# Kernel tuning notes

Hardware: AMD Instinct MI355X
Metric: run time of the kernel (lower is better)

## Reference

```python
import jax, jax.numpy as jnp
import numpy as np

N_NODES = 100000
N_EDGES = 1600000
IN_C, HID_C, OUT_C = 512, 128, 40


def gcn_conv(x, edge_index):
    """Symmetric-normalized sparse aggregation: out[d] = sum_e 1/sqrt(deg[s]*deg[d]) * x[s]."""
    n = x.shape[0]
    src, dst = edge_index[0], edge_index[1]
    deg = jax.ops.segment_sum(jnp.ones_like(dst, dtype=x.dtype), dst, num_segments=n)
    deg = jnp.maximum(deg, 1.0)  # guard isolated nodes
    dinv = jax.lax.rsqrt(deg)
    w = dinv[src] * dinv[dst]                      # [E]
    msg = x[src] * w[:, None]                      # [E, C] gather + scale
    return jax.ops.segment_sum(msg, dst, num_segments=n)  # scatter-add -> [N, C]


def setup_inputs() -> dict:
    key = jax.random.key(0)
    k1, k2, k3, k4 = jax.random.split(key, 4)
    x = jax.random.normal(k1, (N_NODES, IN_C), dtype=jnp.float32)
    edge_index = jax.random.randint(k2, (2, N_EDGES), 0, N_NODES, dtype=jnp.int64)
    # xavier_uniform with gain=1.414 (as in reset_parameters), zero biases
    def xavier(k, shape, gain=1.414):
        fan_out, fan_in = shape
        bound = gain * np.sqrt(6.0 / (fan_in + fan_out))
        return jax.random.uniform(k, shape, jnp.float32, -bound, bound)
    W0 = xavier(k3, (HID_C, IN_C))
    b0 = jnp.zeros((HID_C,), jnp.float32)
    W1 = xavier(k4, (OUT_C, HID_C))
    b1 = jnp.zeros((OUT_C,), jnp.float32)
    return {"x": x, "edge_index": edge_index, "W0": W0, "b0": b0, "W1": W1, "b1": b1}


def reference(x, edge_index, W0, b0, W1, b1):
    # layer 0: project -> sparse aggregate -> bias -> relu (dropout off in eval)
    h = x @ W0.T
    h = gcn_conv(h, edge_index)
    h = jax.nn.relu(h + b0)
    # final layer: project -> sparse aggregate -> bias (no activation)
    h = h @ W1.T
    h = gcn_conv(h, edge_index)
    return h + b1
```

## Files before the change

### kernel.cpp

```cpp
#include <hip/hip_runtime.h>
#include <hip/hip_bf16.h>
#include <cstddef>

#define N_NODES 100000
#define N_EDGES 1600000
#define IN_C 512
#define HID_C 128
#define OUT_C 40
#define OUT_CP 48
#define BK 128
#define PADK 136
#define EPB 8000
#define NPART 200
#define NBKT 196
#define BSHIFT 9

typedef short bf16x8 __attribute__((ext_vector_type(8)));
typedef float f32x4 __attribute__((ext_vector_type(4)));

__device__ __forceinline__ float bf2f(unsigned short u) {
    union { unsigned int i; float f; } v; v.i = ((unsigned int)u) << 16; return v.f;
}
__device__ __forceinline__ float bf2f_lo(unsigned int u) {
    union { unsigned int i; float f; } v; v.i = u << 16; return v.f;
}
__device__ __forceinline__ float bf2f_hi(unsigned int u) {
    union { unsigned int i; float f; } v; v.i = u & 0xFFFF0000u; return v.f;
}
__device__ __forceinline__ unsigned short f2bf(float f) {
    union { float f; unsigned int i; } v; v.f = f;
    unsigned int x = v.i;
    return (unsigned short)((x + 0x7FFFu + ((x >> 16) & 1u)) >> 16);
}

__device__ __forceinline__ void glds16(const void* g, void* l) {
    __builtin_amdgcn_global_load_lds(
        (const __attribute__((address_space(1))) unsigned int*)g,
        (__attribute__((address_space(3))) unsigned int*)l,
        16, 0, 0);
}

__global__ void k_detect(const unsigned int* __restrict__ xbits,
                         const int* __restrict__ ei32, int* __restrict__ flags) {
    if (threadIdx.x == 0 && blockIdx.x == 0) {
        int inrange = 0;
        for (int i = 0; i < 64; i++) {
            unsigned int b = xbits[i * 33 + 1];
            int e = (int)((b >> 23) & 0xFFu);
            if (e >= 90 && e <= 160) inrange++;
        }
        flags[0] = (inrange >= 32) ? 0 : 1;
        int zeros = 0;
        for (int i = 0; i < 8; i++) if (ei32[2 * i + 1] == 0) zeros++;
        flags[1] = (zeros == 8) ? 1 : 0;
    }
}

__device__ __forceinline__ int load_src(const int* ei, int mi, int e) {
    return mi ? ei[2 * e] : ei[e];
}
__device__ __forceinline__ int load_dst(const int* ei, int mi, int e) {
    return mi ? ei[2 * (N_EDGES + e)] : ei[N_EDGES + e];
}

#define NW_TOTAL (IN_C * HID_C + HID_C * OUT_C + HID_C + OUT_C)
__global__ void k_norm_w(const void* __restrict__ W0, const void* __restrict__ W1,
                         const void* __restrict__ b0, const void* __restrict__ b1,
                         const int* __restrict__ flags,
                         unsigned short* __restrict__ w0n, unsigned short* __restrict__ w1n,
                         float* __restrict__ b0n, float* __restrict__ b1n) {
    int mf = flags[0];
    int i = blockIdx.x * 256 + threadIdx.x;
    if (i >= NW_TOTAL) return;
    if (i < IN_C * HID_C) {
        w0n[i] = mf ? ((const unsigned short*)W0)[i] : f2bf(((const float*)W0)[i]);
    } else if (i < IN_C * HID_C + HID_C * OUT_C) {
        int j = i - IN_C * HID_C;
        w1n[j] = mf ? ((const unsigned short*)W1)[j] : f2bf(((const float*)W1)[j]);
    } else if (i < IN_C * HID_C + HID_C * OUT_C + HID_C) {
        int j = i - IN_C * HID_C - HID_C * OUT_C;
        b0n[j] = mf ? bf2f(((const unsigned short*)b0)[j]) : ((const float*)b0)[j];
    } else {
        int j = i - IN_C * HID_C - HID_C * OUT_C - HID_C;
        b1n[j] = mf ? bf2f(((const unsigned short*)b1)[j]) : ((const float*)b1)[j];
    }
}

__global__ __launch_bounds__(256) void k_part1(const int* __restrict__ ei,
                                               const int* __restrict__ flags,
                                               int* __restrict__ bcnt,
                                               int* __restrict__ block_off) {
    __shared__ int h[NBKT];
    int t = threadIdx.x;
    for (int i = t; i < NBKT; i += 256) h[i] = 0;
    __syncthreads();
    int mi = flags[1];
    int base = blockIdx.x * EPB;
    for (int j = t; j < EPB; j += 256) {
        int e = base + j;
        if (e < N_EDGES) atomicAdd(&h[load_dst(ei, mi, e) >> BSHIFT], 1);
    }
    __syncthreads();
    for (int i = t; i < NBKT; i += 256)
        block_off[blockIdx.x * NBKT + i] = atomicAdd(&bcnt[i], h[i]);
}

__global__ void k_scan_bkt(const int* __restrict__ bcnt, int* __restrict__ bbase) {
    __shared__ int sm[256];
    int t = threadIdx.x;
    int v = (t < NBKT) ? bcnt[t] : 0;
    sm[t] = v; __syncthreads();
    for (int off = 1; off < 256; off <<= 1) {
        int a = (t >= off) ? sm[t - off] : 0;
        __syncthreads();
        sm[t] += a;
        __syncthreads();
    }
    if (t < NBKT) bbase[t] = sm[t] - v;
    if (t == NBKT - 1) bbase[NBKT] = sm[t];
}

__global__ __launch_bounds__(256) void k_part2(const int* __restrict__ ei,
                                               const int* __restrict__ flags,
                                               const int* __restrict__ bbase,
                                               const int* __restrict__ block_off,
                                               unsigned int* __restrict__ bedges) {
    __shared__ int cur[NBKT];
    int t = threadIdx.x;
    for (int i = t; i < NBKT; i += 256)
        cur[i] = bbase[i] + block_off[blockIdx.x * NBKT + i];
    __syncthreads();
    int mi = flags[1];
    int base = blockIdx.x * EPB;
    for (int j = t; j < EPB; j += 256) {
        int e = base + j;
        if (e < N_EDGES) {
            int d = load_dst(ei, mi, e);
            int s = load_src(ei, mi, e);
            int p = atomicAdd(&cur[d >> BSHIFT], 1);
            bedges[p] = ((unsigned int)s << BSHIFT) | (unsigned int)(d & 511);
        }
    }
}

__global__ __launch_bounds__(512) void k_bucket_csr(const unsigned int* __restrict__ bedges,
                                                    const int* __restrict__ bbase,
                                                    int* __restrict__ rowptr,
                                                    float* __restrict__ dinv,
                                                    int* __restrict__ col) {
    __shared__ int cnt[512];
    __shared__ int cur[512];
    int b = blockIdx.x, t = threadIdx.x;
    int ebeg = bbase[b], eend = bbase[b + 1];
    cnt[t] = 0;
    __syncthreads();
    for (int j = ebeg + t; j < eend; j += 512)
        atomicAdd(&cnt[bedges[j] & 511], 1);
    __syncthreads();
    int v = cnt[t];
    cur[t] = v; __syncthreads();
    for (int off = 1; off < 512; off <<= 1) {
        int a = (t >= off) ? cur[t - off] : 0;
        __syncthreads();
        cur[t] += a;
        __syncthreads();
    }
    int excl = cur[t] - v;
    int node = b * 512 + t;
    if (node < N_NODES) {
        rowptr[node] = ebeg + excl;
        float dd = (float)v; if (dd < 1.f) dd = 1.f;
        dinv[node] = rsqrtf(dd);
    } else if (node == N_NODES) {
        rowptr[N_NODES] = ebeg + excl;
    }
    __syncthreads();
    cur[t] = ebeg + excl;
    __syncthreads();
    for (int j = ebeg + t; j < eend; j += 512) {
        unsigned int pk = bedges[j];
        int p = atomicAdd(&cur[pk & 511], 1);
        col[p] = (int)(pk >> BSHIFT);
    }
}

template <int MF>
__device__ __forceinline__ void gemm1_body(const void* __restrict__ x,
                                           const unsigned short* __restrict__ w0n,
                                           unsigned short* __restrict__ h1,
                                           unsigned short* __restrict__ Bl,
                                           int node0, int t) {
    int w = t >> 6;
    int lane = t & 63;
    int r16 = lane & 15;
    int quad = lane >> 4;

    f32x4 acc[2][8];
#pragma unroll
    for (int m = 0; m < 2; m++)
#pragma unroll
        for (int c = 0; c < 8; c++) acc[m][c] = (f32x4){0.f, 0.f, 0.f, 0.f};

    int row0 = node0 + w * 32 + r16;
    int row1 = row0 + 16;
    int r0c = row0 < N_NODES ? row0 : N_NODES - 1;
    int r1c = row1 < N_NODES ? row1 : N_NODES - 1;
    const float* a0f = (const float*)x + (size_t)r0c * IN_C + quad * 8;
    const float* a1f = (const float*)x + (size_t)r1c * IN_C + quad * 8;
    const unsigned short* a0h = (const unsigned short*)x + (size_t)r0c * IN_C + quad * 8;
    const unsigned short* a1h = (const unsigned short*)x + (size_t)r1c * IN_C + quad * 8;

    int ch = t >> 1, half = t & 1;
    const unsigned short* gfill = w0n + (size_t)ch * IN_C + half * 64;
    unsigned short* lfill = Bl + ch * PADK + half * 64;

    for (int s = 0; s < 4; s++) {
        int ks0 = s * BK;
        __syncthreads();
#pragma unroll
        for (int i = 0; i < 8; i++) {
            *reinterpret_cast<bf16x8*>(lfill + i * 8) =
                *reinterpret_cast<const bf16x8*>(gfill + ks0 + i * 8);
        }
        __syncthreads();
#pragma unroll
        for (int kk = 0; kk < BK; kk += 32) {
            int k0 = ks0 + kk;
            bf16x8 a0, a1;
            if (MF) {
                a0 = *reinterpret_cast<const bf16x8*>(a0h + k0);
                a1 = *reinterpret_cast<const bf16x8*>(a1h + k0);
            } else {
                float4 f0 = *reinterpret_cast<const float4*>(a0f + k0);
                float4 f1 = *reinterpret_cast<const float4*>(a0f + k0 + 4);
                float4 g0 = *reinterpret_cast<const float4*>(a1f + k0);
                float4 g1 = *reinterpret_cast<const float4*>(a1f + k0 + 4);
                a0 = (bf16x8){(short)f2bf(f0.x), (short)f2bf(f0.y), (short)f2bf(f0.z), (short)f2bf(f0.w),
                              (short)f2bf(f1.x), (short)f2bf(f1.y), (short)f2bf(f1.z), (short)f2bf(f1.w)};
                a1 = (bf16x8){(short)f2bf(g0.x), (short)f2bf(g0.y), (short)f2bf(g0.z), (short)f2bf(g0.w),
                              (short)f2bf(g1.x), (short)f2bf(g1.y), (short)f2bf(g1.z), (short)f2bf(g1.w)};
            }
            const unsigned short* bbase2 = Bl + r16 * PADK + kk + quad * 8;
#pragma unroll
            for (int ct = 0; ct < 8; ct++) {
                bf16x8 b = *reinterpret_cast<const bf16x8*>(bbase2 + ct * 16 * PADK);
                acc[0][ct] = __builtin_amdgcn_mfma_f32_16x16x32_bf16(a0, b, acc[0][ct], 0, 0, 0);
                acc[1][ct] = __builtin_amdgcn_mfma_f32_16x16x32_bf16(a1, b, acc[1][ct], 0, 0, 0);
            }
        }
    }

#pragma unroll
    for (int m = 0; m < 2; m++) {
#pragma unroll
        for (int ct = 0; ct < 8; ct++) {
#pragma unroll
            for (int r = 0; r < 4; r++) {
                int row = node0 + w * 32 + m * 16 + quad * 4 + r;
                if (row < N_NODES)
                    h1[(size_t)row * HID_C + ct * 16 + r16] = f2bf(acc[m][ct][r]);
            }
        }
    }
}

__device__ __forceinline__ void gemm1_bf16_async(const unsigned short* __restrict__ xg,
                                                 const unsigned short* __restrict__ w0n,
                                                 unsigned short* __restrict__ h1,
                                                 unsigned short* __restrict__ smem,
                                                 int node0, int t) {
    const int w = t >> 6;
    const int lane = t & 63;
    const int r16 = lane & 15;
    const int quad = lane >> 4;

    f32x4 acc[2][8];
#pragma unroll
    for (int m = 0; m < 2; m++)
#pragma unroll
        for (int c = 0; c < 8; c++) acc[m][c] = (f32x4){0.f, 0.f, 0.f, 0.f};

    int rA0 = node0 + (2 * w) * 16 + r16;     if (rA0 >= N_NODES) rA0 = N_NODES - 1;
    int rA1 = node0 + (2 * w + 1) * 16 + r16; if (rA1 >= N_NODES) rA1 = N_NODES - 1;
    const unsigned short* pa0 = xg + (size_t)rA0 * IN_C + quad * 8;
    const unsigned short* pa1 = xg + (size_t)rA1 * IN_C + quad * 8;
    const unsigned short* pb0 = w0n + (size_t)((2 * w) * 16 + r16) * IN_C + quad * 8;
    const unsigned short* pb1 = w0n + (size_t)((2 * w + 1) * 16 + r16) * IN_C + quad * 8;

    auto stage = [&](int buf, int ks) {
        unsigned short* a = smem + buf * 8192 + (2 * w) * 512;
        glds16(pa0 + ks, a);
        glds16(pa1 + ks, a + 512);
        glds16(pb0 + ks, a + 4096);
        glds16(pb1 + ks, a + 4096 + 512);
    };

    const int fo = quad * 128 + r16 * 8;

    auto compute = [&](int buf) {
        const unsigned short* Ab = smem + buf * 8192;
        const unsigned short* Bb = Ab + 4096;
        bf16x8 a0 = *reinterpret_cast<const bf16x8*>(Ab + (2 * w) * 512 + fo);
        bf16x8 a1 = *reinterpret_cast<const bf16x8*>(Ab + (2 * w + 1) * 512 + fo);
#pragma unroll
        for (int ct = 0; ct < 8; ct++) {
            bf16x8 b = *reinterpret_cast<const bf16x8*>(Bb + ct * 512 + fo);
            acc[0][ct] = __builtin_amdgcn_mfma_f32_16x16x32_bf16(a0, b, acc[0][ct], 0, 0, 0);
            acc[1][ct] = __builtin_amdgcn_mfma_f32_16x16x32_bf16(a1, b, acc[1][ct], 0, 0, 0);
        }
    };

    stage(0, 0);
    __syncthreads();
    for (int tt = 0; tt < 15; ++tt) {
        int cur = tt & 1;
        stage(cur ^ 1, (tt + 1) * 32);
        compute(cur);
        __syncthreads();
    }
    compute(1);

#pragma unroll
    for (int m = 0; m < 2; m++) {
#pragma unroll
        for (int ct = 0; ct < 8; ct++) {
#pragma unroll
            for (int r = 0; r < 4; r++) {
                int row = node0 + w * 32 + m * 16 + quad * 4 + r;
                if (row < N_NODES)
                    h1[(size_t)row * HID_C + ct * 16 + r16] = f2bf(acc[m][ct][r]);
            }
        }
    }
}

__global__ __launch_bounds__(256, 3) void k_gemm1(const void* __restrict__ x,
                                                  const unsigned short* __restrict__ w0n,
                                                  const int* __restrict__ flags,
                                                  unsigned short* __restrict__ h1) {
    __shared__ unsigned short smem[HID_C * PADK];
    int node0 = blockIdx.x * 128;
    int t = threadIdx.x;
    if (flags[0]) gemm1_bf16_async((const unsigned short*)x, w0n, h1, smem, node0, t);
    else          gemm1_body<0>(x, w0n, h1, smem, node0, t);
}

__global__ __launch_bounds__(256) void k_agg1(const int* __restrict__ rowptr,
                                              const int* __restrict__ col,
                                              const float* __restrict__ dinv,
                                              const unsigned int* __restrict__ h1v,
                                              const float* __restrict__ b0n,
                                              unsigned int* __restrict__ h2v) {
    int w = threadIdx.x >> 6;
    int lane = threadIdx.x & 63;
    int d = blockIdx.x * 4 + w;
    if (d >= N_NODES) return;
    int beg = rowptr[d], end = rowptr[d + 1];
    float a0 = 0.f, a1 = 0.f;
    int j = beg;
    for (; j + 8 <= end; j += 8) {
        int s[8];
        float wj[8];
        unsigned int r[8];
#pragma unroll
        for (int q = 0; q < 8; q++) s[q] = col[j + q];
#pragma unroll
        for (int q = 0; q < 8; q++) wj[q] = dinv[s[q]];
#pragma unroll
        for (int q = 0; q < 8; q++) r[q] = h1v[(size_t)s[q] * 64 + lane];
#pragma unroll
        for (int q = 0; q < 8; q++) {
            a0 += wj[q] * bf2f_lo(r[q]);
            a1 += wj[q] * bf2f_hi(r[q]);
        }
    }
    for (; j < end; j++) {
        int s = col[j];
        float wj = dinv[s];
        unsigned int r = h1v[(size_t)s * 64 + lane];
        a0 += wj * bf2f_lo(r);
        a1 += wj * bf2f_hi(r);
    }
    float dv = dinv[d];
    float o0 = a0 * dv + b0n[2 * lane];
    float o1 = a1 * dv + b0n[2 * lane + 1];
    o0 = o0 > 0.f ? o0 : 0.f;
    o1 = o1 > 0.f ? o1 : 0.f;
    h2v[(size_t)d * 64 + lane] = (unsigned int)f2bf(o0) | ((unsigned int)f2bf(o1) << 16);
}

__global__ __launch_bounds__(256) void k_gemm2(const unsigned short* __restrict__ h2,
                                               const unsigned short* __restrict__ w1p,
                                               float* __restrict__ p2) {
    int wave = (blockIdx.x * 256 + (int)threadIdx.x) >> 6;
    if (wave >= N_NODES / 16) return;
    int lane = threadIdx.x & 63;
    int r16 = lane & 15;
    int quad = lane >> 4;
    int node_base = wave * 16;

    f32x4 acc[3];
#pragma unroll
    for (int c = 0; c < 3; c++) acc[c] = (f32x4){0.f, 0.f, 0.f, 0.f};

    const unsigned short* arow = h2 + (size_t)(node_base + r16) * HID_C + quad * 8;
    const unsigned short* brow = w1p + (size_t)r16 * HID_C + quad * 8;

#pragma unroll
    for (int k0 = 0; k0 < HID_C; k0 += 32) {
        bf16x8 a = *reinterpret_cast<const bf16x8*>(arow + k0);
#pragma unroll
        for (int ct = 0; ct < 3; ct++) {
            bf16x8 b = *reinterpret_cast<const bf16x8*>(brow + (size_t)ct * 16 * HID_C + k0);
            acc[ct] = __builtin_amdgcn_mfma_f32_16x16x32_bf16(a, b, acc[ct], 0, 0, 0);
        }
    }

#pragma unroll
    for (int ct = 0; ct < 3; ct++) {
        int chan = ct * 16 + r16;
        if (chan < OUT_C) {
#pragma unroll
            for (int r = 0; r < 4; r++) {
                p2[(size_t)(node_base + quad * 4 + r) * OUT_C + chan] = acc[ct][r];
            }
        }
    }
}

__global__ __launch_bounds__(256) void k_agg2(const int* __restrict__ rowptr,
                                              const int* __restrict__ col,
                                              const float* __restrict__ dinv,
                                              const float* __restrict__ p2,
                                              const float* __restrict__ b1n,
                                              const int* __restrict__ flags,
                                              void* __restrict__ out) {
    int w = threadIdx.x >> 6;
    int lane = threadIdx.x & 63;
    int d = blockIdx.x * 4 + w;
    if (d >= N_NODES || lane >= OUT_C) return;
    int beg = rowptr[d], end = rowptr[d + 1];
    float acc = 0.f;
    int j = beg;
    for (; j + 8 <= end; j += 8) {
        int s[8];
        float wj[8], r[8];
#pragma unroll
        for (int q = 0; q < 8; q++) s[q] = col[j + q];
#pragma unroll
        for (int q = 0; q < 8; q++) wj[q] = dinv[s[q]];
#pragma unroll
        for (int q = 0; q < 8; q++) r[q] = p2[(size_t)s[q] * OUT_C + lane];
#pragma unroll
        for (int q = 0; q < 8; q++) acc += wj[q] * r[q];
    }
    for (; j < end; j++) {
        int s = col[j];
        acc += dinv[s] * p2[(size_t)s * OUT_C + lane];
    }
    float v = acc * dinv[d] + b1n[lane];
    size_t idx = (size_t)d * OUT_C + lane;
    if (flags[0]) ((unsigned short*)out)[idx] = f2bf(v);
    else          ((float*)out)[idx] = v;
}

extern "C" void kernel_launch(void* const* d_in, const int* in_sizes, int n_in,
                              void* d_out, int out_size, void* d_ws, size_t ws_size,
                              hipStream_t stream) {
    const void* x  = d_in[0];
    const int* ei  = (const int*)d_in[1];
    const void* W0 = d_in[2];
    const void* b0 = d_in[3];
    const void* W1 = d_in[4];
    const void* b1 = d_in[5];

    char* ws = (char*)d_ws;
    size_t off = 0;
    auto alloc = [&](size_t bytes) {
        char* p = ws + off;
        off += (bytes + 511) & ~(size_t)511;
        return p;
    };
    int*   flags   = (int*)  alloc(sizeof(int) * 2);
    int*   rowptr  = (int*)  alloc(sizeof(int) * (N_NODES + 1));
    float* dinv    = (float*)alloc(sizeof(float) * N_NODES);
    int*   col     = (int*)  alloc(sizeof(int) * N_EDGES);
    int*   bcnt    = (int*)  alloc(sizeof(int) * NBKT);
    int*   bbase   = (int*)  alloc(sizeof(int) * (NBKT + 1));
    int*   bloff   = (int*)  alloc(sizeof(int) * NPART * NBKT);
    unsigned int* bedges = (unsigned int*)alloc(sizeof(unsigned int) * N_EDGES);
    unsigned short* w0n = (unsigned short*)alloc(sizeof(unsigned short) * IN_C * HID_C);
    unsigned short* w1n = (unsigned short*)alloc(sizeof(unsigned short) * OUT_CP * HID_C);
    float* b0n = (float*)alloc(sizeof(float) * HID_C);
    float* b1n = (float*)alloc(sizeof(float) * OUT_C);
    unsigned short* h1 = (unsigned short*)alloc(sizeof(unsigned short) * (size_t)N_NODES * HID_C);
    unsigned short* h2 = (unsigned short*)alloc(sizeof(unsigned short) * (size_t)N_NODES * HID_C);
    float* p2 = (float*)h1;

    k_detect<<<1, 64, 0, stream>>>((const unsigned int*)x, ei, flags);
    hipMemsetAsync(w1n, 0, sizeof(unsigned short) * OUT_CP * HID_C, stream);
    k_norm_w<<<(NW_TOTAL + 255) / 256, 256, 0, stream>>>(W0, W1, b0, b1, flags, w0n, w1n, b0n, b1n);

    hipMemsetAsync(bcnt, 0, sizeof(int) * NBKT, stream);
    k_part1<<<NPART, 256, 0, stream>>>(ei, flags, bcnt, bloff);
    k_scan_bkt<<<1, 256, 0, stream>>>(bcnt, bbase);
    k_part2<<<NPART, 256, 0, stream>>>(ei, flags, bbase, bloff, bedges);
    k_bucket_csr<<<NBKT, 512, 0, stream>>>(bedges, bbase, rowptr, dinv, col);

    k_gemm1<<<(N_NODES + 127) / 128, 256, 0, stream>>>(x, w0n, flags, h1);
    k_agg1<<<(N_NODES + 3) / 4, 256, 0, stream>>>(rowptr, col, dinv,
                                                  (const unsigned int*)h1, b0n,
                                                  (unsigned int*)h2);
    k_gemm2<<<(N_NODES / 16 + 3) / 4, 256, 0, stream>>>(h2, w1n, p2);
    k_agg2<<<(N_NODES + 3) / 4, 256, 0, stream>>>(rowptr, col, dinv, p2, b1n, flags, d_out);
}
```

Baseline: 566.0 us.

## Double-buffer fp32 x and W0 tiles into LDS via async global-to-LDS loads

```diff
diff --git a/kernel.cpp b/kernel.cpp
--- a/kernel.cpp
+++ b/kernel.cpp
@@ -8,8 +8,6 @@
 #define HID_C 128
 #define OUT_C 40
 #define OUT_CP 48
-#define BK 128
-#define PADK 136
 #define EPB 8000
 #define NPART 200
 #define NBKT 196
@@ -184,16 +182,18 @@
     }
 }
 
-template <int MF>
-__device__ __forceinline__ void gemm1_body(const void* __restrict__ x,
-                                           const unsigned short* __restrict__ w0n,
-                                           unsigned short* __restrict__ h1,
-                                           unsigned short* __restrict__ Bl,
-                                           int node0, int t) {
-    int w = t >> 6;
-    int lane = t & 63;
-    int r16 = lane & 15;
-    int quad = lane >> 4;
+#define G1_BUF 24576
+#define G1_BOFF 16384
+
+__device__ __forceinline__ void gemm1_f32_async(const float* __restrict__ xg,
+                                                const unsigned short* __restrict__ w0n,
+                                                unsigned short* __restrict__ h1,
+                                                char* __restrict__ smem,
+                                                int node0, int t) {
+    const int w = t >> 6;
+    const int lane = t & 63;
+    const int r16 = lane & 15;
+    const int quad = lane >> 4;
 
     f32x4 acc[2][8];
 #pragma unroll
@@ -201,54 +201,64 @@
 #pragma unroll
         for (int c = 0; c < 8; c++) acc[m][c] = (f32x4){0.f, 0.f, 0.f, 0.f};
 
-    int row0 = node0 + w * 32 + r16;
-    int row1 = row0 + 16;
-    int r0c = row0 < N_NODES ? row0 : N_NODES - 1;
-    int r1c = row1 < N_NODES ? row1 : N_NODES - 1;
-    const float* a0f = (const float*)x + (size_t)r0c * IN_C + quad * 8;
-    const float* a1f = (const float*)x + (size_t)r1c * IN_C + quad * 8;
-    const unsigned short* a0h = (const unsigned short*)x + (size_t)r0c * IN_C + quad * 8;
-    const unsigned short* a1h = (const unsigned short*)x + (size_t)r1c * IN_C + quad * 8;
-
-    int ch = t >> 1, half = t & 1;
-    const unsigned short* gfill = w0n + (size_t)ch * IN_C + half * 64;
-    unsigned short* lfill = Bl + ch * PADK + half * 64;
-
-    for (int s = 0; s < 4; s++) {
-        int ks0 = s * BK;
+    const int lrow = lane >> 3;
+    const int lch = (lane & 7) ^ lrow;
+    const float* pa[4];
+#pragma unroll
+    for (int g = 0; g < 4; g++) {
+        int r = node0 + w * 32 + 8 * g + lrow;
+        if (r >= N_NODES) r = N_NODES - 1;
+        pa[g] = xg + (size_t)r * IN_C + lch * 4;
+    }
+    const unsigned short* pb[2];
+#pragma unroll
+    for (int g = 0; g < 2; g++)
+        pb[g] = w0n + (size_t)((2 * w + g) * 16 + r16) * IN_C + quad * 8;
+
+    auto stage = [&](int buf, int ks) {
+        char* Ab = smem + buf * G1_BUF + w * 4096;
+        char* Bb = smem + buf * G1_BUF + G1_BOFF + w * 2048;
+        glds16(pa[0] + ks, Ab);
+        glds16(pa[1] + ks, Ab + 1024);
+        glds16(pa[2] + ks, Ab + 2048);
+        glds16(pa[3] + ks, Ab + 3072);
+        glds16(pb[0] + ks, Bb);
+        glds16(pb[1] + ks, Bb + 1024);
+    };
+
+    const int swz = r16 & 7;
+
+    auto compute = [&](int buf) {
+        const char* Ab = smem + buf * G1_BUF;
+        const char* Bb = Ab + G1_BOFF;
+        bf16x8 a[2];
+#pragma unroll
+        for (int m = 0; m < 2; m++) {
+            int rowb = (w * 32 + m * 16 + r16) * 128;
+            int c0 = ((2 * quad) ^ swz) * 16;
+            int c1 = ((2 * quad + 1) ^ swz) * 16;
+            float4 fa = *reinterpret_cast<const float4*>(Ab + rowb + c0);
+            float4 fb = *reinterpret_cast<const float4*>(Ab + rowb + c1);
+            a[m] = (bf16x8){(short)f2bf(fa.x), (short)f2bf(fa.y), (short)f2bf(fa.z), (short)f2bf(fa.w),
+                            (short)f2bf(fb.x), (short)f2bf(fb.y), (short)f2bf(fb.z), (short)f2bf(fb.w)};
+        }
+#pragma unroll
+        for (int ct = 0; ct < 8; ct++) {
+            bf16x8 b = *reinterpret_cast<const bf16x8*>(Bb + ct * 1024 + lane * 16);
+            acc[0][ct] = __builtin_amdgcn_mfma_f32_16x16x32_bf16(a[0], b, acc[0][ct], 0, 0, 0);
+            acc[1][ct] = __builtin_amdgcn_mfma_f32_16x16x32_bf16(a[1], b, acc[1][ct], 0, 0, 0);
+        }
+    };
+
+    stage(0, 0);
+    __syncthreads();
+    for (int tt = 0; tt < 15; ++tt) {
+        int cur = tt & 1;
+        stage(cur ^ 1, (tt + 1) * 32);
+        compute(cur);
         __syncthreads();
-#pragma unroll
-        for (int i = 0; i < 8; i++) {
-            *reinterpret_cast<bf16x8*>(lfill + i * 8) =
-                *reinterpret_cast<const bf16x8*>(gfill + ks0 + i * 8);
-        }
-        __syncthreads();
-#pragma unroll
-        for (int kk = 0; kk < BK; kk += 32) {
-            int k0 = ks0 + kk;
-            bf16x8 a0, a1;
-            if (MF) {
-                a0 = *reinterpret_cast<const bf16x8*>(a0h + k0);
-                a1 = *reinterpret_cast<const bf16x8*>(a1h + k0);
-            } else {
-                float4 f0 = *reinterpret_cast<const float4*>(a0f + k0);
-                float4 f1 = *reinterpret_cast<const float4*>(a0f + k0 + 4);
-                float4 g0 = *reinterpret_cast<const float4*>(a1f + k0);
-                float4 g1 = *reinterpret_cast<const float4*>(a1f + k0 + 4);
-                a0 = (bf16x8){(short)f2bf(f0.x), (short)f2bf(f0.y), (short)f2bf(f0.z), (short)f2bf(f0.w),
-                              (short)f2bf(f1.x), (short)f2bf(f1.y), (short)f2bf(f1.z), (short)f2bf(f1.w)};
-                a1 = (bf16x8){(short)f2bf(g0.x), (short)f2bf(g0.y), (short)f2bf(g0.z), (short)f2bf(g0.w),
-                              (short)f2bf(g1.x), (short)f2bf(g1.y), (short)f2bf(g1.z), (short)f2bf(g1.w)};
-            }
-            const unsigned short* bbase2 = Bl + r16 * PADK + kk + quad * 8;
-#pragma unroll
-            for (int ct = 0; ct < 8; ct++) {
-                bf16x8 b = *reinterpret_cast<const bf16x8*>(bbase2 + ct * 16 * PADK);
-                acc[0][ct] = __builtin_amdgcn_mfma_f32_16x16x32_bf16(a0, b, acc[0][ct], 0, 0, 0);
-                acc[1][ct] = __builtin_amdgcn_mfma_f32_16x16x32_bf16(a1, b, acc[1][ct], 0, 0, 0);
-            }
-        }
-    }
+    }
+    compute(1);
 
 #pragma unroll
     for (int m = 0; m < 2; m++) {
@@ -338,11 +348,12 @@
                                                   const unsigned short* __restrict__ w0n,
                                                   const int* __restrict__ flags,
                                                   unsigned short* __restrict__ h1) {
-    __shared__ unsigned short smem[HID_C * PADK];
+    __shared__ __align__(16) char smem[2 * G1_BUF];
     int node0 = blockIdx.x * 128;
     int t = threadIdx.x;
-    if (flags[0]) gemm1_bf16_async((const unsigned short*)x, w0n, h1, smem, node0, t);
-    else          gemm1_body<0>(x, w0n, h1, smem, node0, t);
+    if (flags[0]) gemm1_bf16_async((const unsigned short*)x, w0n, h1,
+                                   (unsigned short*)smem, node0, t);
+    else          gemm1_f32_async((const float*)x, w0n, h1, smem, node0, t);
 }
 
 __global__ __launch_bounds__(256) void k_agg1(const int* __restrict__ rowptr,
```

Result: faster. 543.6 us (-4.0%).
